# Kernel tuning notes

Measured on AMD Instinct MI355X. Metric: run time of the kernel, lower is better.

## Reference

```python
import jax, jax.numpy as jnp
import numpy as np

_SAMPLING_EPS = 1e-5


def setup_inputs() -> dict:
    key = jax.random.key(0)
    k1, k2, k3, k4, k5 = jax.random.split(key, 5)
    B, V = 128, 128000
    logits = jax.random.normal(k1, (B, V), dtype=jnp.float32)
    temperature = jax.random.uniform(k2, (B,), dtype=jnp.float32)
    top_k = jax.random.randint(k3, (B,), 0, 1024)
    top_p = jax.random.uniform(k4, (B,), dtype=jnp.float32)
    # uniform noise -> exponential via -log(u) inside reference (torch's q.exponential_())
    q = jnp.clip(jax.random.uniform(k5, (B, V), dtype=jnp.float32), 1e-10, 1.0)
    return {"logits": logits, "temperature": temperature, "top_k": top_k,
            "top_p": top_p, "q": q, "max_num_logprobs": 5}


def reference(logits, temperature, top_k, top_p, q, max_num_logprobs):
    B, V = logits.shape
    # apply_temperature: temp < eps treated as 1.0 (greedy rows untouched)
    temp = jnp.where(temperature < _SAMPLING_EPS, 1.0, temperature)
    logits = logits.astype(jnp.float32) / temp[:, None]

    # _apply_top_k_top_p: ascending sort over vocab
    idx = jnp.argsort(logits, axis=-1)                      # [B, V]
    ls = jnp.take_along_axis(logits, idx, axis=-1)          # sorted ascending
    k = jnp.clip(top_k.astype(jnp.int32), 1, V)
    thr = jnp.take_along_axis(ls, (V - k)[:, None], axis=-1)  # k-th largest value
    ls = jnp.where(ls < thr, -jnp.inf, ls)
    # top-p on the top-k-masked sorted logits
    ps = jax.nn.softmax(ls, axis=-1)
    cum = jnp.cumsum(ps, axis=-1)
    p_mask = cum <= (1.0 - top_p)[:, None]
    p_mask = p_mask.at[:, -1].set(False)
    ls = jnp.where(p_mask, -jnp.inf, ls)
    # scatter masked sorted logits back to original vocab positions
    rows = jnp.arange(B)[:, None]
    logits = jnp.zeros_like(logits).at[rows, idx].set(ls)

    # get_probs + sample
    probs = jax.nn.softmax(logits, axis=-1)
    e = -jnp.log(q)                                         # exponential noise
    greedy = jnp.argmax(probs, axis=-1)
    rand = jnp.argmax(probs / e, axis=-1)                   # Gumbel-max equivalent
    sampled = jnp.where(temperature < _SAMPLING_EPS, greedy, rand).astype(jnp.int32)

    # top-k logprobs
    logprobs = jax.nn.log_softmax(logits, axis=-1)
    topk_logprobs, topk_indices = jax.lax.top_k(logprobs, max_num_logprobs)
    return sampled, topk_logprobs, topk_indices.astype(jnp.int32)
```

## Files before the change

kernel.cpp:

```cpp
#include <hip/hip_runtime.h>
#include <math.h>
#include <float.h>

typedef unsigned long long u64;
typedef unsigned u32;

#define NT 1024
#define NW 16
#define NT1 256
#define SL 8
#define NB 8192
#define BSH 19
#define NBM 4096
#define CAP 2048
#define EPT4 8
#define SUB2 64
#define TOPN 5
#define SCALE_D 17592186044416.0
#define NEG_BIG -3.0e38f

#define ADDRT(g) ((((g) & 15u) << 8) | ((g) >> 4))

struct RowCtl { u32 kb; u32 cnt0; u32 maxKey; u32 rin; u32 bail; u32 pad[27]; };

__device__ __forceinline__ u32 key_of(float f){
  u32 u = __float_as_uint(f);
  return (u & 0x80000000u) ? ~u : (u | 0x80000000u);
}
__device__ __forceinline__ float key_to_float(u32 k){
  u32 u = (k & 0x80000000u) ? (k & 0x7FFFFFFFu) : ~k;
  return __uint_as_float(u);
}
__device__ __forceinline__ u64 quantMass(float l, float m){
  float ef = expf(l - m);
  return (u64)((double)ef * SCALE_D + 0.5);
}

struct Top5 { float v[TOPN]; int ix[TOPN]; };
__device__ __forceinline__ void t5_init(Top5& t){
  for (int j=0;j<TOPN;j++){ t.v[j] = -INFINITY; t.ix[j] = 0x7FFFFFFF; }
}
__device__ __forceinline__ void t5_insert(Top5& t, float nv, int ni){
  for (int j=0;j<TOPN;j++){
    if (nv > t.v[j] || (nv == t.v[j] && ni < t.ix[j])){
      for (int s=TOPN-1;s>j;s--){ t.v[s]=t.v[s-1]; t.ix[s]=t.ix[s-1]; }
      t.v[j]=nv; t.ix[j]=ni;
      return;
    }
  }
}

__device__ void scan_excl(u64* arr, int n, u64* wsum){
  const int tid = threadIdx.x, lane = tid & 63, w = tid >> 6;
  __syncthreads();
  const int chunk = (n + NT - 1) / NT;
  const int base = tid * chunk;
  u64 local = 0;
  for (int j=0;j<chunk;j++){ int i=base+j; if (i<n) local += arr[i]; }
  u64 inc = local;
  for (int off=1; off<64; off<<=1){
    u64 up = __shfl_up(inc, off, 64);
    if (lane >= off) inc += up;
  }
  if (lane == 63) wsum[w] = inc;
  __syncthreads();
  if (tid == 0){
    u64 acc = 0;
    for (int i=0;i<NW;i++){ u64 v = wsum[i]; wsum[i] = acc; acc += v; }
    arr[n] = acc;
  }
  __syncthreads();
  u64 run = wsum[w] + (inc - local);
  for (int j=0;j<chunk;j++){ int i=base+j; if (i<n){ u64 v=arr[i]; arr[i]=run; run += v; } }
  __syncthreads();
}


__global__ void k0_zero(u32* __restrict__ hist, u32* __restrict__ ctlw, int Bn){
  size_t n = (size_t)Bn * NB;
  size_t stride = (size_t)gridDim.x * blockDim.x;
  for (size_t i = (size_t)blockIdx.x*blockDim.x + threadIdx.x; i < n; i += stride) hist[i] = 0;
  size_t nc = (size_t)Bn * (sizeof(RowCtl)/4);
  for (size_t i = (size_t)blockIdx.x*blockDim.x + threadIdx.x; i < nc; i += stride) ctlw[i] = 0;
}

__global__ __launch_bounds__(NT1) void k1_hist(const float* __restrict__ L,
        const float* __restrict__ temp, u32* __restrict__ hist, RowCtl* __restrict__ ctl,
        int Bn, int Vn){
  __shared__ u32 lh[NB];
  const int b = blockIdx.y, s = blockIdx.x, tid = threadIdx.x;
  for (int j=tid;j<NB;j+=NT1) lh[j]=0;
  const float tr = temp[b]; const float tEff = (tr < 1e-5f) ? 1.0f : tr;
  const float* Lr = L + (size_t)b*Vn;
  const int chunk = (Vn + SL-1)/SL;
  const int i0 = s*chunk, i1 = min(i0+chunk, Vn);
  __syncthreads();
  const int nv = (i1 - i0) / 4;
  const float4* L4 = (const float4*)(Lr + i0);
  u32 mk = 0;
  for (int v=tid; v<nv; v+=NT1){
    float4 x = L4[v];
    #pragma unroll
    for (int e=0;e<4;e++){
      float l = (&x.x)[e] / tEff;
      u32 k = key_of(l);
      atomicAdd(&lh[k>>BSH], 1u);
      mk = max(mk, k);
    }
  }
  for (int i=i0+nv*4+tid; i<i1; i+=NT1){
    float l = Lr[i]/tEff;
    u32 k = key_of(l);
    atomicAdd(&lh[k>>BSH], 1u);
    mk = max(mk, k);
  }
  for (int off=32; off; off>>=1){ u32 o=__shfl_xor(mk,off,64); mk=max(mk,o); }
  if ((tid&63)==0) atomicMax(&ctl[b].maxKey, mk);
  __syncthreads();
  u32* Hr = hist + (size_t)b*NB;
  for (int j=tid;j<NB;j+=NT1){ u32 c = lh[j]; if (c) atomicAdd(&Hr[j], c); }
}

__global__ __launch_bounds__(NT) void k2_kb(const int* __restrict__ top_k,
        const u32* __restrict__ hist, RowCtl* __restrict__ ctl, int Bn, int Vn){
  __shared__ u32 sh[NB+1];
  __shared__ u32 wsum[NW];
  __shared__ int s_g;
  __shared__ u32 s_base;
  const int b = blockIdx.x, tid = threadIdx.x, lane = tid&63, w = tid>>6;
  const u32* Hr = hist + (size_t)b*NB;
  for (int j=tid;j<NB;j+=NT) sh[j] = Hr[j];
  __syncthreads();
  const int chunk = NB/NT;
  u32 local=0;
  for (int j=0;j<chunk;j++) local += sh[tid*chunk+j];
  u32 inc = local;
  for (int off=1;off<64;off<<=1){ u32 up=__shfl_up(inc,off,64); if (lane>=off) inc+=up; }
  if (lane==63) wsum[w]=inc;
  __syncthreads();
  if (tid==0){ u32 acc=0; for(int i=0;i<NW;i++){u32 v=wsum[i]; wsum[i]=acc; acc+=v;} sh[NB]=acc; }
  __syncthreads();
  u32 run = wsum[w] + (inc - local);
  for (int j=0;j<chunk;j++){ int i2=tid*chunk+j; u32 v=sh[i2]; sh[i2]=run; run+=v; }
  __syncthreads();
  int kk = top_k[b]; if (kk<1) kk=1; if (kk>Vn) kk=Vn;
  const u32 rank = (u32)(Vn - kk);
  for (int j=tid;j<NB;j+=NT) if (sh[j] <= rank && rank < sh[j+1]){ s_g = j; s_base = sh[j]; }
  __syncthreads();
  if (tid==0){ ctl[b].kb = (u32)s_g; ctl[b].rin = rank - s_base; }
}

__global__ __launch_bounds__(NT1) void k3_collect(const float* __restrict__ L,
        const float* __restrict__ temp, u64* __restrict__ cand, RowCtl* __restrict__ ctl,
        int Bn, int Vn){
  const int b = blockIdx.y, s = blockIdx.x, tid = threadIdx.x;
  const float tr = temp[b]; const float tEff = (tr<1e-5f)?1.0f:tr;
  const u32 kbMinKey = ctl[b].kb << BSH;
  const float* Lr = L + (size_t)b*Vn;
  u64* Cr = cand + (size_t)b*CAP;
  const int chunk = (Vn + SL-1)/SL;
  const int i0 = s*chunk, i1 = min(i0+chunk, Vn);
  const int nv = (i1 - i0) / 4;
  const float4* L4 = (const float4*)(Lr + i0);
  const int lane = tid & 63;
  for (int v=tid; v<nv; v+=NT1){
    float4 x = L4[v];
    #pragma unroll
    for (int e=0;e<4;e++){
      float l = (&x.x)[e] / tEff;
      u32 k = key_of(l);
      bool pred = (k >= kbMinKey);
      u64 mk = __ballot(pred);
      if (mk){
        int leader = __ffsll((long long)mk) - 1;
        u32 base = 0;
        if (lane == leader) base = atomicAdd(&ctl[b].cnt0, (u32)__popcll(mk));
        base = __shfl(base, leader, 64);
        if (pred){
          u32 p = base + (u32)__popcll(mk & ((1ull<<lane)-1ull));
          if (p < CAP) Cr[p] = ((u64)k<<32) | (u64)(u32)(i0 + v*4 + e);
        }
      }
    }
  }
  for (int i=i0+nv*4+tid; i<i1; i+=NT1){
    float l = Lr[i]/tEff;
    u32 k = key_of(l);
    if (k >= kbMinKey){
      u32 p = atomicAdd(&ctl[b].cnt0, 1u);
      if (p < CAP) Cr[p] = ((u64)k<<32) | (u64)(u32)i;
    }
  }
}

__global__ __launch_bounds__(NT1) void k4_solve(const float* __restrict__ L,
        const float* __restrict__ temp, const int* __restrict__ top_k,
        const float* __restrict__ top_p, const float* __restrict__ qn,
        const u64* __restrict__ cand, RowCtl* __restrict__ ctl,
        float* __restrict__ out, int Bn, int Vn){
  __shared__ u32 cnt[NBM];
  __shared__ u64 mass[NBM];
  __shared__ u64 sub[SUB2];
  __shared__ u64 msub[SUB2];
  __shared__ u32 wsc[4];
  __shared__ u64 wsm[4];
  __shared__ int s_cnt, s_bail, s_ga, s_gb;
  __shared__ u32 s_thr, s_r3;
  __shared__ u64 s_Pgb;
  __shared__ float s_fill[16];
  __shared__ Top5 s_wt5[4];
  __shared__ double s_wr[4];
  __shared__ int s_wri[4], s_wg[4];
  __shared__ u64 s_ms[4], s_pb[4];

  const int b = blockIdx.x, tid = threadIdx.x, lane = tid&63, w = tid>>6;
  const u32 n0raw = ctl[b].cnt0;
  if (n0raw == 0 || n0raw > CAP) return;
  const int n0 = (int)n0raw;
  const float tr = temp[b]; const float tEff = (tr<1e-5f)?1.0f:tr;
  const float* Lr = L + (size_t)b*Vn;
  const float* Qr = qn + (size_t)b*Vn;
  const u64* Cr = cand + (size_t)b*CAP;
  const u32 kb = ctl[b].kb;
  const u32 rin = ctl[b].rin;
  const u32 mKey = ctl[b].maxKey;
  const float m = key_to_float(mKey);

  for (int i=tid;i<NBM;i+=NT1){ cnt[i]=0; mass[i]=0; }
  if (tid==0){ s_cnt=0; s_bail=0; s_ga=0; s_gb=0; s_r3=0; s_Pgb=0; }
  if (tid<16) s_fill[tid] = (tid<Vn) ? Lr[tid] : 0.f;
  u64 pr[EPT4]; u32 kk_[EPT4]; bool vd[EPT4];
  #pragma unroll
  for (int e=0;e<EPT4;e++){
    int p = tid + e*NT1;
    vd[e] = (p < n0);
    pr[e] = vd[e] ? Cr[p] : ~0ull;
    kk_[e] = (u32)(pr[e]>>32);
  }
  __syncthreads();

  bool inkb[EPT4]; u32 binA[EPT4];
  #pragma unroll
  for (int e=0;e<EPT4;e++){
    inkb[e] = vd[e] && ((kk_[e]>>BSH) == kb);
    binA[e] = (kk_[e] & 0x7FFFFu) >> 7;
    if (inkb[e]) atomicAdd(&cnt[ADDRT(binA[e])], 1u);
  }
  __syncthreads();
  {
    u32 c16[16]; u32 lsum = 0;
    #pragma unroll
    for (int j=0;j<16;j++){ c16[j] = cnt[(j<<8)|tid]; lsum += c16[j]; }
    u32 inc = lsum;
    for (int off=1;off<64;off<<=1){ u32 up=__shfl_up(inc,off,64); if (lane>=off) inc+=up; }
    if (lane==63) wsc[w] = inc;
    __syncthreads();
    u32 wb = 0;
    for (int i=0;i<4;i++) if (i<w) wb += wsc[i];
    u32 run = wb + inc - lsum;
    #pragma unroll
    for (int j=0;j<16;j++){
      if (run <= rin && rin < run + c16[j]){ s_ga = tid*16+j; s_r3 = rin - run; }
      run += c16[j];
    }
  }
  __syncthreads();
  const int ga = s_ga;
  const u32 r3 = s_r3;
  #pragma unroll
  for (int e=0;e<EPT4;e++){
    if (inkb[e] && (int)binA[e] == ga){
      int p = atomicAdd(&s_cnt, 1);
      if (p < SUB2) sub[p] = pr[e]; else s_bail = 1;
    }
  }
  __syncthreads();
  if (s_bail){ if (tid==0) ctl[b].bail = 1; return; }
  const int ncolA = min(s_cnt, SUB2);
  for (int t=tid; t<ncolA; t+=NT1){
    u64 own = sub[t]; u32 rk = 0;
    for (int j=0;j<ncolA;j++) rk += (sub[j] < own);
    if (rk == r3) s_thr = (u32)(own>>32);
  }
  __syncthreads();
  const u32 thrKey = s_thr;

  u64 ms_[EPT4];
  const u32 span = mKey - thrKey;
  int shb = 0;
  if (span > 4095u){ int hb = 31 - __clz(span); shb = hb - 11; }
  u32 binB[EPT4];
  if (tid==0) s_cnt = 0;
  #pragma unroll
  for (int e=0;e<EPT4;e++){
    ms_[e] = (vd[e] && kk_[e] >= thrKey) ? quantMass(key_to_float(kk_[e]), m) : 0ull;
    binB[e] = ms_[e] ? ((kk_[e] - thrKey) >> shb) : 0u;
    if (ms_[e]) atomicAdd(&mass[ADDRT(binB[e])], ms_[e]);
  }
  __syncthreads();
  u64 Qq = 0, Tt = 0;
  {
    u64 m16[16]; u64 lsm = 0;
    #pragma unroll
    for (int j=0;j<16;j++){ m16[j] = mass[(j<<8)|tid]; lsm += m16[j]; }
    u64 incm = lsm;
    for (int off=1;off<64;off<<=1){ u64 up=__shfl_up(incm,off,64); if (lane>=off) incm+=up; }
    if (lane==63) wsm[w] = incm;
    __syncthreads();
    u64 wbm = 0, T = 0;
    for (int i=0;i<4;i++){ T += wsm[i]; if (i<w) wbm += wsm[i]; }
    const float cf = 1.0f - top_p[b];
    u64 Q = (u64)((double)cf * (double)T);
    if (Q >= T) Q = T - 1;
    u64 run = wbm + incm - lsm;
    #pragma unroll
    for (int j=0;j<16;j++){
      if (run <= Q && Q < run + m16[j]){ s_gb = tid*16+j; s_Pgb = run; }
      run += m16[j];
    }
    Qq = Q; Tt = T;
  }
  __syncthreads();
  const int gb = s_gb;
  const u64 Pgb = s_Pgb;
  const u64 Q = Qq, T = Tt;
  #pragma unroll
  for (int e=0;e<EPT4;e++){
    if (ms_[e] && (int)binB[e] == gb){
      int p = atomicAdd(&s_cnt, 1);
      if (p < SUB2){ sub[p] = pr[e]; msub[p] = ms_[e]; } else s_bail = 1;
    }
  }
  __syncthreads();
  if (s_bail){ if (tid==0) ctl[b].bail = 1; return; }
  const int ncolB = min(s_cnt, SUB2);
  u64 cacc[EPT4];
  bool inb[EPT4];
  #pragma unroll
  for (int e=0;e<EPT4;e++){ cacc[e]=0; inb[e] = (ms_[e] != 0) && ((int)binB[e] == gb); }
  for (int j=0;j<ncolB;j++){
    u64 pj = sub[j]; u64 mj = msub[j];
    #pragma unroll
    for (int e=0;e<EPT4;e++)
      if (inb[e] && pj < pr[e]) cacc[e] += mj;
  }
  bool sv[EPT4];
  u64 mm = 0; u64 pb = ~0ull;
  #pragma unroll
  for (int e=0;e<EPT4;e++){
    bool masked = false;
    if (ms_[e]){
      if ((int)binB[e] < gb) masked = true;
      else if ((int)binB[e] == gb && (Pgb + cacc[e] + ms_[e]) <= Q) masked = true;
    }
    sv[e] = (ms_[e] != 0) && !masked;
    if (masked) mm += ms_[e];
    if (sv[e] && pr[e] < pb) pb = pr[e];
  }

  float qv[EPT4];
  #pragma unroll
  for (int e=0;e<EPT4;e++) qv[e] = sv[e] ? Qr[(u32)pr[e]] : 1.0f;
  Top5 t5; t5_init(t5);
  double br = -1.0; int bri = 0x7FFFFFFF; int gmin = 0x7FFFFFFF;
  #pragma unroll
  for (int e=0;e<EPT4;e++){
    if (sv[e]){
      float l = key_to_float(kk_[e]); int idx = (int)(u32)pr[e];
      double ratio = (double)expf(l - m) / (double)(-logf(qv[e]));
      if (ratio > br || (ratio == br && idx < bri)){ br = ratio; bri = idx; }
      if (kk_[e] == mKey && idx < gmin) gmin = idx;
      t5_insert(t5, l, idx);
    }
  }
  for (int off=1; off<64; off<<=1){
    Top5 o;
    for (int j=0;j<TOPN;j++){ o.v[j]=__shfl_xor(t5.v[j],off,64); o.ix[j]=__shfl_xor(t5.ix[j],off,64); }
    for (int j=0;j<TOPN;j++) t5_insert(t5, o.v[j], o.ix[j]);
    double orr = __shfl_xor(br, off, 64); int ori = __shfl_xor(bri, off, 64);
    if (orr > br || (orr == br && ori < bri)){ br = orr; bri = ori; }
    int og = __shfl_xor(gmin, off, 64); if (og < gmin) gmin = og;
    mm += __shfl_xor(mm, off, 64);
    u64 op = __shfl_xor(pb, off, 64); if (op < pb) pb = op;
  }
  if (lane==0){ s_wt5[w]=t5; s_wr[w]=br; s_wri[w]=bri; s_wg[w]=gmin; s_ms[w]=mm; s_pb[w]=pb; }
  __syncthreads();
  if (tid==0){
    Top5 f = s_wt5[0];
    double fr = s_wr[0]; int fri = s_wri[0]; int fg = s_wg[0];
    u64 fms = s_ms[0]; u64 fpb = s_pb[0];
    for (int wi=1; wi<4; wi++){
      for (int j=0;j<TOPN;j++) t5_insert(f, s_wt5[wi].v[j], s_wt5[wi].ix[j]);
      if (s_wr[wi] > fr || (s_wr[wi]==fr && s_wri[wi]<fri)){ fr=s_wr[wi]; fri=s_wri[wi]; }
      if (s_wg[wi] < fg) fg = s_wg[wi];
      fms += s_ms[wi];
      if (s_pb[wi] < fpb) fpb = s_pb[wi];
    }
    const u64 S2 = T - fms;
    int filled = 0;
    for (int i=0; i<16 && i<Vn && filled<TOPN; i++){
      float l = s_fill[i]/tEff;
      u64 pr2 = ((u64)key_of(l)<<32) | (u64)(u32)i;
      if (pr2 < fpb){ t5_insert(f, -INFINITY, i); filled++; }
    }
    double lS = log((double)S2 / SCALE_D);
    int sampled = (tr < 1e-5f) ? fg : fri;
    out[b] = (float)sampled;
    for (int j=0;j<TOPN;j++){
      float lv = f.v[j];
      float lp = (lv == -INFINITY) ? NEG_BIG : (float)((double)lv - (double)m - lS);
      out[Bn + b*TOPN + j] = lp;
      out[Bn + Bn*TOPN + b*TOPN + j] = (float)f.ix[j];
    }
  }
}


__device__ void find_cross(const u64* arr, int n, u64 target, int* s_fh, u64* s_fb){
  const int tid = threadIdx.x;
  const int chunk = (n + NT - 1) / NT;
  const int base = tid * chunk;
  for (int j=0;j<chunk;j++){
    int i = base + j;
    if (i < n && arr[i] <= target && target < arr[i+1]){ *s_fh = i; *s_fb = arr[i]; }
  }
  __syncthreads();
}

__device__ void fallback_row(int b, const float* logits, const float* temperature,
                             const int* top_k, const float* top_p, const float* qnoise,
                             float* out, int Bn, int Vn){
  __shared__ u64 s_hist[4097];
  __shared__ u64 s_wsum[NW];
  __shared__ int s_fh;
  __shared__ u64 s_fb;
  __shared__ float s_fm[NW];
  __shared__ float s_m;
  __shared__ int s_lastMax;
  __shared__ int s_eqcnt;
  __shared__ int s_eqlist[1024];
  __shared__ int s_sel;
  __shared__ Top5 s_wt5[NW];
  __shared__ double s_wr[NW];
  __shared__ int s_wri[NW];
  __shared__ int s_wg[NW];
  __shared__ u64 s_ws2[NW];

  const int tid = threadIdx.x, lane = tid & 63, w = tid >> 6;
  const float* L  = logits + (size_t)b * Vn;
  const float* Qr = qnoise + (size_t)b * Vn;
  const float tRaw = temperature[b];
  const float tEff = (tRaw < 1e-5f) ? 1.0f : tRaw;

  for (int i=tid;i<4097;i+=NT) s_hist[i] = 0;
  if (tid==0){ s_lastMax = -1; s_eqcnt = 0; }
  __syncthreads();
  float lm = -INFINITY;
  for (int i=tid;i<Vn;i+=NT){
    float l = L[i] / tEff;
    u32 k = key_of(l);
    atomicAdd(&s_hist[k>>20], 1ull);
    lm = fmaxf(lm, l);
  }
  for (int off=32; off; off>>=1) lm = fmaxf(lm, __shfl_xor(lm, off, 64));
  if (lane==0) s_fm[w] = lm;
  scan_excl(s_hist, 4096, s_wsum);
  if (tid==0){ float mm=-INFINITY; for (int i=0;i<NW;i++) mm=fmaxf(mm,s_fm[i]); s_m=mm; }
  __syncthreads();
  const float m = s_m;

  int kk = top_k[b]; if (kk < 1) kk = 1; if (kk > Vn) kk = Vn;
  u64 r = (u64)(Vn - kk);
  find_cross(s_hist, 4096, r, &s_fh, &s_fb);
  const int kb0 = s_fh; r -= s_fb;
  __syncthreads();

  for (int i=tid;i<4097;i+=NT) s_hist[i]=0;
  __syncthreads();
  for (int i=tid;i<Vn;i+=NT){
    float l = L[i]/tEff; u32 k = key_of(l);
    if ((int)(k>>20) == kb0) atomicAdd(&s_hist[(k>>8)&0xFFFu], 1ull);
  }
  scan_excl(s_hist, 4096, s_wsum);
  find_cross(s_hist, 4096, r, &s_fh, &s_fb);
  const int kb1 = s_fh; r -= s_fb;
  __syncthreads();

  const u32 ktop24 = ((u32)kb0<<12) | (u32)kb1;
  for (int i=tid;i<4097;i+=NT) s_hist[i]=0;
  __syncthreads();
  for (int i=tid;i<Vn;i+=NT){
    float l = L[i]/tEff; u32 k = key_of(l);
    if ((k>>8) == ktop24) atomicAdd(&s_hist[k & 0xFFu], 1ull);
  }
  scan_excl(s_hist, 256, s_wsum);
  find_cross(s_hist, 256, r, &s_fh, &s_fb);
  const u32 thrKey = (ktop24<<8) | (u32)s_fh;
  const float thr = key_to_float(thrKey);
  __syncthreads();

  for (int i=tid;i<4097;i+=NT) s_hist[i]=0;
  __syncthreads();
  for (int i=tid;i<Vn;i+=NT){
    float l = L[i]/tEff;
    if (l >= thr){
      u32 k = key_of(l);
      double sd = exp((double)l - (double)m);
      u64 qv = (u64)(sd * SCALE_D + 0.5);
      atomicAdd(&s_hist[k>>20], qv);
      if (l == m) atomicMax(&s_lastMax, i);
    }
  }
  scan_excl(s_hist, 4096, s_wsum);
  const u64 T = s_hist[4096];
  const float cf = 1.0f - top_p[b];
  const double qtd = (double)cf * (double)T;
  u64 Qfix = (qtd >= (double)T) ? T : (u64)qtd;
  const bool allmask = (Qfix >= T);

  u32 vKey = 0xFFFFFFFFu;
  int idxStar = 0x7FFFFFFF;

  if (!allmask){
    find_cross(s_hist, 4096, Qfix, &s_fh, &s_fb);
    const int g0 = s_fh;
    u64 Qrem = Qfix - s_fb;
    __syncthreads();

    for (int i=tid;i<4097;i+=NT) s_hist[i]=0;
    __syncthreads();
    for (int i=tid;i<Vn;i+=NT){
      float l = L[i]/tEff;
      if (l >= thr){
        u32 k = key_of(l);
        if ((int)(k>>20) == g0){
          double sd = exp((double)l - (double)m);
          atomicAdd(&s_hist[(k>>8)&0xFFFu], (u64)(sd*SCALE_D+0.5));
        }
      }
    }
    scan_excl(s_hist, 4096, s_wsum);
    find_cross(s_hist, 4096, Qrem, &s_fh, &s_fb);
    const int g1 = s_fh; Qrem -= s_fb;
    __syncthreads();

    const u32 ptop24 = ((u32)g0<<12)|(u32)g1;
    for (int i=tid;i<4097;i+=NT) s_hist[i]=0;
    __syncthreads();
    for (int i=tid;i<Vn;i+=NT){
      float l = L[i]/tEff;
      if (l >= thr){
        u32 k = key_of(l);
        if ((k>>8) == ptop24){
          double sd = exp((double)l - (double)m);
          atomicAdd(&s_hist[k & 0xFFu], (u64)(sd*SCALE_D+0.5));
        }
      }
    }
    scan_excl(s_hist, 256, s_wsum);
    find_cross(s_hist, 256, Qrem, &s_fh, &s_fb);
    const int g2 = s_fh;
    const u64 base2 = s_fb;
    const u64 nextPref = s_hist[g2+1];
    Qrem -= base2;
    vKey = (ptop24<<8) | (u32)g2;
    const float vStar = key_to_float(vKey);
    const double sv = exp((double)vStar - (double)m);
    const u64 qstar = (u64)(sv*SCALE_D+0.5);
    u64 nstar = (qstar > 0) ? (nextPref - base2) / qstar : 1ull;
    if (nstar < 1) nstar = 1;
    u64 tmask = (qstar > 0) ? (Qrem / qstar) : 0ull;
    if (tmask >= nstar) tmask = nstar - 1;
    idxStar = -1;
    __syncthreads();
    if (tmask >= 1){
      for (int i=tid;i<Vn;i+=NT){
        float l = L[i]/tEff;
        if (key_of(l) == vKey){
          int p = atomicAdd(&s_eqcnt, 1);
          if (p < 1024) s_eqlist[p] = i;
        }
      }
      __syncthreads();
      if (tid == 0){
        int n_ = s_eqcnt; if (n_ > 1024) n_ = 1024;
        for (int a=1;a<n_;a++){
          int key0 = s_eqlist[a]; int c2=a-1;
          while (c2>=0 && s_eqlist[c2]>key0){ s_eqlist[c2+1]=s_eqlist[c2]; c2--; }
          s_eqlist[c2+1]=key0;
        }
        int ti = (int)tmask - 1;
        if (ti >= n_) ti = n_-1;
        s_sel = s_eqlist[ti];
      }
      __syncthreads();
      idxStar = s_sel;
    }
  }

  const int lastMax = s_lastMax;
  Top5 t5; t5_init(t5);
  u64 s2 = 0;
  double br = -1.0; int bri = 0x7FFFFFFF;
  int gmin = 0x7FFFFFFF;
  for (int i=tid;i<Vn;i+=NT){
    float l = L[i]/tEff;
    u32 k = key_of(l);
    bool surv = (l >= thr) &&
                ((k > vKey) || (k == vKey && i > idxStar) || (i == lastMax));
    float val;
    if (surv){
      double sd = exp((double)l - (double)m);
      s2 += (u64)(sd*SCALE_D+0.5);
      float u = expf(l - m);
      float e = -logf(Qr[i]);
      double ratio = (double)u / (double)e;
      if (ratio > br || (ratio == br && i < bri)){ br = ratio; bri = i; }
      if (l == m && i < gmin) gmin = i;
      val = l;
    } else {
      val = -INFINITY;
    }
    t5_insert(t5, val, i);
  }
  for (int off=1; off<64; off<<=1){
    Top5 o;
    for (int j=0;j<TOPN;j++){ o.v[j]=__shfl_xor(t5.v[j],off,64); o.ix[j]=__shfl_xor(t5.ix[j],off,64); }
    for (int j=0;j<TOPN;j++) t5_insert(t5, o.v[j], o.ix[j]);
    double orr = __shfl_xor(br, off, 64);
    int ori = __shfl_xor(bri, off, 64);
    if (orr > br || (orr == br && ori < bri)){ br = orr; bri = ori; }
    int og = __shfl_xor(gmin, off, 64); if (og < gmin) gmin = og;
    s2 += __shfl_xor(s2, off, 64);
  }
  if (lane == 0){
    s_wt5[w] = t5; s_wr[w]=br; s_wri[w]=bri; s_wg[w]=gmin; s_ws2[w]=s2;
  }
  __syncthreads();
  if (tid == 0){
    Top5 f = s_wt5[0];
    double fr = s_wr[0]; int fri = s_wri[0]; int fg = s_wg[0];
    u64 fs2 = s_ws2[0];
    for (int wi=1; wi<NW; wi++){
      for (int j=0;j<TOPN;j++) t5_insert(f, s_wt5[wi].v[j], s_wt5[wi].ix[j]);
      if (s_wr[wi] > fr || (s_wr[wi]==fr && s_wri[wi]<fri)){ fr=s_wr[wi]; fri=s_wri[wi]; }
      if (s_wg[wi] < fg) fg = s_wg[wi];
      fs2 += s_ws2[wi];
    }
    double S2d = (double)fs2 / SCALE_D;
    double lS = log(S2d);
    int sampled = (tRaw < 1e-5f) ? fg : fri;
    out[b] = (float)sampled;
    for (int j=0;j<TOPN;j++){
      float lv = f.v[j];
      float lp = (lv == -INFINITY) ? NEG_BIG : (float)((double)lv - (double)m - lS);
      out[Bn + b*TOPN + j] = lp;
      out[Bn + Bn*TOPN + b*TOPN + j] = (float)f.ix[j];
    }
  }
}

__global__ __launch_bounds__(NT) void k5_rowfb(const float* __restrict__ logits,
        const float* __restrict__ temperature, const int* __restrict__ top_k,
        const float* __restrict__ top_p, const float* __restrict__ qnoise,
        const RowCtl* __restrict__ ctl, float* __restrict__ out, int Bn, int Vn){
  const int b = blockIdx.x;
  const u32 c = ctl[b].cnt0;
  if (c > 0 && c <= CAP && !ctl[b].bail) return;
  fallback_row(b, logits, temperature, top_k, top_p, qnoise, out, Bn, Vn);
}

extern "C" __global__ void __launch_bounds__(NT)
sampler_fallback(const float* __restrict__ logits, const float* __restrict__ temperature,
                 const int* __restrict__ top_k, const float* __restrict__ top_p,
                 const float* __restrict__ qnoise, float* __restrict__ out, int Bn, int Vn){
  fallback_row(blockIdx.x, logits, temperature, top_k, top_p, qnoise, out, Bn, Vn);
}


extern "C" void kernel_launch(void* const* d_in, const int* in_sizes, int n_in,
                              void* d_out, int out_size, void* d_ws, size_t ws_size,
                              hipStream_t stream)
{
  const float* logits      = (const float*)d_in[0];
  const float* temperature = (const float*)d_in[1];
  const int*   top_k       = (const int*)d_in[2];
  const float* top_p       = (const float*)d_in[3];
  const float* q           = (const float*)d_in[4];
  const int Bn = in_sizes[1];
  const int Vn = in_sizes[0] / Bn;

  const size_t offCand = (size_t)Bn * NB * 4;
  const size_t offCtl  = offCand + (size_t)Bn * CAP * 8;
  const size_t total   = offCtl + (size_t)Bn * sizeof(RowCtl);

  if (ws_size < total){
    sampler_fallback<<<dim3(Bn), dim3(NT), 0, stream>>>(
        logits, temperature, top_k, top_p, q, (float*)d_out, Bn, Vn);
    return;
  }

  char* wsb = (char*)d_ws;
  u32*    hist = (u32*)wsb;
  u64*    cand = (u64*)(wsb + offCand);
  RowCtl* ctl  = (RowCtl*)(wsb + offCtl);

  k0_zero   <<<dim3(512),     dim3(256), 0, stream>>>(hist, (u32*)ctl, Bn);
  k1_hist   <<<dim3(SL, Bn),  dim3(NT1), 0, stream>>>(logits, temperature, hist, ctl, Bn, Vn);
  k2_kb     <<<dim3(Bn),      dim3(NT),  0, stream>>>(top_k, hist, ctl, Bn, Vn);
  k3_collect<<<dim3(SL, Bn),  dim3(NT1), 0, stream>>>(logits, temperature, cand, ctl, Bn, Vn);
  k4_solve  <<<dim3(Bn),      dim3(NT1), 0, stream>>>(logits, temperature, top_k, top_p, q,
                                                      cand, ctl, (float*)d_out, Bn, Vn);
  k5_rowfb  <<<dim3(Bn),      dim3(NT),  0, stream>>>(logits, temperature, top_k, top_p, q,
                                                      ctl, (float*)d_out, Bn, Vn);
}
```

Before: 130.5 us.

## Merge top-k count and top-p mass histograms into a single pass in solve kernel

The solve kernel now builds the count histogram and the mass histogram together, binning mass over the range from the top-k bucket base to the max key instead of waiting for the exact threshold. It turns the mass histogram into an in-place prefix sum and then corrects for the threshold bin using a block reduction of in-bin surviving mass. This removes one histogram/scan/barrier phase. The random-noise gather is also issued up front for all candidates to overlap its latency. The cost is extra atomics and gathers for non-surviving candidates, plus more complex edge handling around the threshold bin.

```diff
diff --git a/kernel.cpp b/kernel.cpp
--- a/kernel.cpp
+++ b/kernel.cpp
@@ -204,9 +204,9 @@
   __shared__ u64 msub[SUB2];
   __shared__ u32 wsc[4];
   __shared__ u64 wsm[4];
+  __shared__ u64 s_ibs[4];
   __shared__ int s_cnt, s_bail, s_ga, s_gb;
   __shared__ u32 s_thr, s_r3;
-  __shared__ u64 s_Pgb;
   __shared__ float s_fill[16];
   __shared__ Top5 s_wt5[4];
   __shared__ double s_wr[4];
@@ -224,12 +224,13 @@
   const u32 kb = ctl[b].kb;
   const u32 rin = ctl[b].rin;
   const u32 mKey = ctl[b].maxKey;
+  const u32 kbMin = kb << BSH;
   const float m = key_to_float(mKey);
 
   for (int i=tid;i<NBM;i+=NT1){ cnt[i]=0; mass[i]=0; }
-  if (tid==0){ s_cnt=0; s_bail=0; s_ga=0; s_gb=0; s_r3=0; s_Pgb=0; }
+  if (tid==0){ s_cnt=0; s_bail=0; s_ga=0; s_gb=0; s_r3=0; }
   if (tid<16) s_fill[tid] = (tid<Vn) ? Lr[tid] : 0.f;
-  u64 pr[EPT4]; u32 kk_[EPT4]; bool vd[EPT4];
+  u64 pr[EPT4]; u32 kk_[EPT4]; bool vd[EPT4]; float qv[EPT4];
   #pragma unroll
   for (int e=0;e<EPT4;e++){
     int p = tid + e*NT1;
@@ -237,36 +238,55 @@
     pr[e] = vd[e] ? Cr[p] : ~0ull;
     kk_[e] = (u32)(pr[e]>>32);
   }
-  __syncthreads();
-
-  bool inkb[EPT4]; u32 binA[EPT4];
+  #pragma unroll
+  for (int e=0;e<EPT4;e++) qv[e] = vd[e] ? Qr[(u32)pr[e]] : 1.0f;
+
+  const u32 span = mKey - kbMin;
+  int shb = 0; if (span > 4095u){ int hb = 31 - __clz(span); shb = hb - 11; }
+  u64 msA[EPT4]; u32 binA[EPT4], binM[EPT4]; bool inkb[EPT4];
   #pragma unroll
   for (int e=0;e<EPT4;e++){
     inkb[e] = vd[e] && ((kk_[e]>>BSH) == kb);
     binA[e] = (kk_[e] & 0x7FFFFu) >> 7;
+    binM[e] = vd[e] ? ((kk_[e] - kbMin) >> shb) : 0u;
+    msA[e]  = vd[e] ? quantMass(key_to_float(kk_[e]), m) : 0ull;
+  }
+  __syncthreads();
+  #pragma unroll
+  for (int e=0;e<EPT4;e++){
     if (inkb[e]) atomicAdd(&cnt[ADDRT(binA[e])], 1u);
-  }
-  __syncthreads();
-  {
-    u32 c16[16]; u32 lsum = 0;
-    #pragma unroll
-    for (int j=0;j<16;j++){ c16[j] = cnt[(j<<8)|tid]; lsum += c16[j]; }
-    u32 inc = lsum;
-    for (int off=1;off<64;off<<=1){ u32 up=__shfl_up(inc,off,64); if (lane>=off) inc+=up; }
-    if (lane==63) wsc[w] = inc;
-    __syncthreads();
-    u32 wb = 0;
-    for (int i=0;i<4;i++) if (i<w) wb += wsc[i];
-    u32 run = wb + inc - lsum;
-    #pragma unroll
-    for (int j=0;j<16;j++){
-      if (run <= rin && rin < run + c16[j]){ s_ga = tid*16+j; s_r3 = rin - run; }
-      run += c16[j];
-    }
-  }
-  __syncthreads();
-  const int ga = s_ga;
-  const u32 r3 = s_r3;
+    if (vd[e])   atomicAdd(&mass[ADDRT(binM[e])], msA[e]);
+  }
+  __syncthreads();
+
+  u32 c16[16]; u64 m16[16];
+  u32 lsc = 0; u64 lsm = 0;
+  #pragma unroll
+  for (int j=0;j<16;j++){
+    c16[j] = cnt[(j<<8)|tid]; lsc += c16[j];
+    m16[j] = mass[(j<<8)|tid]; lsm += m16[j];
+  }
+  u32 incc = lsc; u64 incm = lsm;
+  for (int off=1;off<64;off<<=1){
+    u32 uc=__shfl_up(incc,off,64); if (lane>=off) incc+=uc;
+    u64 um=__shfl_up(incm,off,64); if (lane>=off) incm+=um;
+  }
+  if (lane==63){ wsc[w]=incc; wsm[w]=incm; }
+  __syncthreads();
+  u32 wbc=0; u64 wbm=0, Tall=0;
+  for (int i=0;i<4;i++){ Tall += wsm[i]; if (i<w){ wbc += wsc[i]; wbm += wsm[i]; } }
+  u32 runc = wbc + incc - lsc;
+  const u64 runm = wbm + incm - lsm;
+  u64 runm2 = runm;
+  #pragma unroll
+  for (int j=0;j<16;j++){
+    if (runc <= rin && rin < runc + c16[j]){ s_ga = tid*16+j; s_r3 = rin - runc; }
+    runc += c16[j];
+    mass[(j<<8)|tid] = runm2;
+    runm2 += m16[j];
+  }
+  __syncthreads();
+  const int ga = s_ga; const u32 r3 = s_r3;
   #pragma unroll
   for (int e=0;e<EPT4;e++){
     if (inkb[e] && (int)binA[e] == ga){
@@ -282,85 +302,75 @@
     for (int j=0;j<ncolA;j++) rk += (sub[j] < own);
     if (rk == r3) s_thr = (u32)(own>>32);
   }
+  if (tid==0) s_cnt = 0;
   __syncthreads();
   const u32 thrKey = s_thr;
-
-  u64 ms_[EPT4];
-  const u32 span = mKey - thrKey;
-  int shb = 0;
-  if (span > 4095u){ int hb = 31 - __clz(span); shb = hb - 11; }
-  u32 binB[EPT4];
-  if (tid==0) s_cnt = 0;
-  #pragma unroll
-  for (int e=0;e<EPT4;e++){
-    ms_[e] = (vd[e] && kk_[e] >= thrKey) ? quantMass(key_to_float(kk_[e]), m) : 0ull;
-    binB[e] = ms_[e] ? ((kk_[e] - thrKey) >> shb) : 0u;
-    if (ms_[e]) atomicAdd(&mass[ADDRT(binB[e])], ms_[e]);
-  }
-  __syncthreads();
-  u64 Qq = 0, Tt = 0;
-  {
-    u64 m16[16]; u64 lsm = 0;
-    #pragma unroll
-    for (int j=0;j<16;j++){ m16[j] = mass[(j<<8)|tid]; lsm += m16[j]; }
-    u64 incm = lsm;
-    for (int off=1;off<64;off<<=1){ u64 up=__shfl_up(incm,off,64); if (lane>=off) incm+=up; }
-    if (lane==63) wsm[w] = incm;
-    __syncthreads();
-    u64 wbm = 0, T = 0;
-    for (int i=0;i<4;i++){ T += wsm[i]; if (i<w) wbm += wsm[i]; }
-    const float cf = 1.0f - top_p[b];
-    u64 Q = (u64)((double)cf * (double)T);
-    if (Q >= T) Q = T - 1;
-    u64 run = wbm + incm - lsm;
+  const int thrBin = (int)((thrKey - kbMin) >> shb);
+
+  u64 ibs = 0;
+  #pragma unroll
+  for (int e=0;e<EPT4;e++)
+    if (vd[e] && (int)binM[e] == thrBin && kk_[e] >= thrKey) ibs += msA[e];
+  for (int off=1;off<64;off<<=1) ibs += __shfl_xor(ibs, off, 64);
+  if (lane==0) s_ibs[w] = ibs;
+  __syncthreads();
+  const u64 inB = s_ibs[0]+s_ibs[1]+s_ibs[2]+s_ibs[3];
+  const u64 prefA = (thrBin >= NBM-1) ? Tall : mass[ADDRT((u32)(thrBin+1))];
+  const u64 T = Tall - prefA + inB;
+  const float cf = 1.0f - top_p[b];
+  u64 Q = (u64)((double)cf * (double)T);
+  if (Q >= T) Q = T - 1;
+  const bool inThr = (Q < inB);
+  const u64 Qp = Q + prefA - inB;
+  if (!inThr){
+    u64 run3 = runm;
     #pragma unroll
     for (int j=0;j<16;j++){
-      if (run <= Q && Q < run + m16[j]){ s_gb = tid*16+j; s_Pgb = run; }
-      run += m16[j];
-    }
-    Qq = Q; Tt = T;
-  }
+      if (run3 <= Qp && Qp < run3 + m16[j]) s_gb = tid*16+j;
+      run3 += m16[j];
+    }
+  } else if (tid==0) s_gb = thrBin;
   __syncthreads();
   const int gb = s_gb;
-  const u64 Pgb = s_Pgb;
-  const u64 Q = Qq, T = Tt;
+  const u64 Pgb = inThr ? 0ull : mass[ADDRT((u32)gb)];
+  const u64 Qd  = inThr ? Q : Qp;
   #pragma unroll
   for (int e=0;e<EPT4;e++){
-    if (ms_[e] && (int)binB[e] == gb){
+    bool f = vd[e] && ((int)binM[e] == gb) && (!inThr || kk_[e] >= thrKey);
+    if (f){
       int p = atomicAdd(&s_cnt, 1);
-      if (p < SUB2){ sub[p] = pr[e]; msub[p] = ms_[e]; } else s_bail = 1;
+      if (p < SUB2){ sub[p] = pr[e]; msub[p] = msA[e]; } else s_bail = 1;
     }
   }
   __syncthreads();
   if (s_bail){ if (tid==0) ctl[b].bail = 1; return; }
   const int ncolB = min(s_cnt, SUB2);
-  u64 cacc[EPT4];
-  bool inb[EPT4];
-  #pragma unroll
-  for (int e=0;e<EPT4;e++){ cacc[e]=0; inb[e] = (ms_[e] != 0) && ((int)binB[e] == gb); }
+  u64 cacc[EPT4]; bool inb[EPT4];
+  #pragma unroll
+  for (int e=0;e<EPT4;e++){
+    inb[e] = vd[e] && ((int)binM[e] == gb) && (!inThr || kk_[e] >= thrKey);
+    cacc[e] = 0;
+  }
   for (int j=0;j<ncolB;j++){
     u64 pj = sub[j]; u64 mj = msub[j];
     #pragma unroll
     for (int e=0;e<EPT4;e++)
       if (inb[e] && pj < pr[e]) cacc[e] += mj;
   }
-  bool sv[EPT4];
-  u64 mm = 0; u64 pb = ~0ull;
+  bool sv[EPT4]; u64 mm = 0; u64 pb = ~0ull;
   #pragma unroll
   for (int e=0;e<EPT4;e++){
+    bool isSurvKey = vd[e] && kk_[e] >= thrKey;
     bool masked = false;
-    if (ms_[e]){
-      if ((int)binB[e] < gb) masked = true;
-      else if ((int)binB[e] == gb && (Pgb + cacc[e] + ms_[e]) <= Q) masked = true;
-    }
-    sv[e] = (ms_[e] != 0) && !masked;
-    if (masked) mm += ms_[e];
+    if (isSurvKey){
+      if ((int)binM[e] < gb) masked = true;
+      else if (inb[e] && (Pgb + cacc[e] + msA[e]) <= Qd) masked = true;
+    }
+    sv[e] = isSurvKey && !masked;
+    if (isSurvKey && masked) mm += msA[e];
     if (sv[e] && pr[e] < pb) pb = pr[e];
   }
 
-  float qv[EPT4];
-  #pragma unroll
-  for (int e=0;e<EPT4;e++) qv[e] = sv[e] ? Qr[(u32)pr[e]] : 1.0f;
   Top5 t5; t5_init(t5);
   double br = -1.0; int bri = 0x7FFFFFFF; int gmin = 0x7FFFFFFF;
   #pragma unroll
```

New measurement: 132.2 us. No clear change (+1.3%).
